# Kernel tuning notes

Hardware: AMD Instinct MI355X
Metric: run time of the kernel (lower is better)

## Reference

```python
import jax, jax.numpy as jnp
import numpy as np

NEG_BIG = 1e13  # matches the torch module's (mask-1)*1e13 additive mask


def setup_inputs() -> dict:
    key = jax.random.key(0)
    k1, k2, k3, k4 = jax.random.split(key, 4)
    B, Lq, Lk, D = 32, 1024, 1024, 1024  # D = 2*hidden = 2*embedding
    query = jax.random.normal(k1, (B, Lq, D), dtype=jnp.float32)
    key_t = jax.random.normal(k2, (B, Lk, D), dtype=jnp.float32)
    key_mask = jax.random.randint(k3, (B, Lk), 0, 2).astype(jnp.float32)
    # Linear(hidden*2 -> embedding*2): weight [out, in] torch convention
    W = jax.random.normal(k4, (D, D), dtype=jnp.float32) * (1.0 / np.sqrt(D))
    b = jnp.zeros((D,), dtype=jnp.float32)
    return {"query": query, "key": key_t, "key_mask": key_mask, "W": W, "b": b}


def reference(query, key, key_mask, W, b):
    # query_emb: Dropout (identity at eval) -> Linear -> ReLU
    query_feat = jax.nn.relu(jnp.einsum("bqd,ed->bqe", query, W) + b)  # [B,Lq,D]
    # bmm with multiplicatively masked key
    masked_key = key * key_mask[:, :, None]                             # [B,Lk,D]
    score = jnp.einsum("bqd,bkd->bqk", query_feat, masked_key)          # [B,Lq,Lk]
    # masked_softmax: score*mask + (mask-1)*1e13, softmax over last dim
    m = key_mask[:, None, :]                                            # [B,1,Lk]
    attn = jax.nn.softmax(score * m + (m - 1.0) * NEG_BIG, axis=-1)     # [B,Lq,Lk]
    # weighted sum over the UNmasked key (as in the original module)
    return jnp.einsum("bqk,bkd->bqd", attn, key)                        # [B,Lq,D]
```

## Files before the change

### kernel.cpp

```cpp
#include <hip/hip_runtime.h>
#include <hip/hip_bf16.h>


typedef __attribute__((ext_vector_type(4))) float f32x4;
typedef __attribute__((ext_vector_type(8))) short s16x8;

#define MFMA16(a, b, c) __builtin_amdgcn_mfma_f32_16x16x32_bf16((a), (b), (c), 0, 0, 0)

__device__ __forceinline__ unsigned short f2bf(float x) {
  unsigned u = __builtin_bit_cast(unsigned, x);
  return (unsigned short)((u + 0x7FFFu + ((u >> 16) & 1u)) >> 16);
}
__device__ __forceinline__ float bf2f(unsigned short h) {
  return __builtin_bit_cast(float, ((unsigned)h) << 16);
}
__device__ __forceinline__ int swz(int row, int col) {
  return (row * 64 + col) ^ ((row & 7) << 3);
}
__device__ __forceinline__ void cvt8(const float* __restrict__ s, s16x8& h8, s16x8& l8) {
  f32x4 a = *(const f32x4*)s;
  f32x4 b = *(const f32x4*)(s + 4);
#pragma unroll
  for (int i = 0; i < 8; i++) {
    float v = (i < 4) ? a[i] : b[i - 4];
    unsigned short hu = f2bf(v);
    unsigned short lu = f2bf(v - bf2f(hu));
    h8[i] = (short)hu;
    l8[i] = (short)lu;
  }
}
__device__ __forceinline__ void gld16(const void* g, void* lds) {
  __builtin_amdgcn_global_load_lds((const __attribute__((address_space(1))) unsigned int*)g,
                                   (__attribute__((address_space(3))) unsigned int*)lds, 16, 0, 0);
}

#define OFF_KHI 0ULL
#define OFF_KLO 67108864ULL
#define OFF_KHIT 134217728ULL
#define OFF_QHI 201326592ULL
#define OFF_QLO 268435456ULL
#define OFF_WHI 335544320ULL
#define OFF_WLO 337641472ULL
#define WS_TIER_A 339738624ULL
#define WS_TIER_B2 201326592ULL

__global__ __launch_bounds__(256) void k_cvt_pair(const float* __restrict__ src,
                                                  unsigned short* __restrict__ hi,
                                                  unsigned short* __restrict__ lo, int n8) {
  int i = blockIdx.x * 256 + threadIdx.x;
  if (i >= n8) return;
  s16x8 h, l;
  cvt8(src + (size_t)i * 8, h, l);
  *(s16x8*)(hi + (size_t)i * 8) = h;
  *(s16x8*)(lo + (size_t)i * 8) = l;
}

__global__ __launch_bounds__(256) void k_cvt_k(const float* __restrict__ K,
                                               unsigned short* __restrict__ Khi,
                                               unsigned short* __restrict__ Klo,
                                               unsigned short* __restrict__ KhiT) {
  __shared__ unsigned T[64 * 65];
  const int t = threadIdx.x;
  const int db0 = blockIdx.x * 64, kb0 = blockIdx.y * 64, b = blockIdx.z;
  const size_t base = (size_t)b * 1024 * 1024;
#pragma unroll
  for (int i = 0; i < 2; i++) {
    const int r = (t >> 3) + i * 32, c0 = (t & 7) * 8;
    s16x8 h, l;
    cvt8(K + base + (size_t)(kb0 + r) * 1024 + db0 + c0, h, l);
    *(s16x8*)(Khi + base + (size_t)(kb0 + r) * 1024 + db0 + c0) = h;
    *(s16x8*)(Klo + base + (size_t)(kb0 + r) * 1024 + db0 + c0) = l;
#pragma unroll
    for (int j = 0; j < 8; j++)
      T[r * 65 + c0 + j] = ((unsigned)(unsigned short)h[j] << 16) | (unsigned short)l[j];
  }
  __syncthreads();
#pragma unroll
  for (int i = 0; i < 2; i++) {
    const int rd = (t >> 3) + i * 32, ck0 = (t & 7) * 8;
    s16x8 h;
#pragma unroll
    for (int j = 0; j < 8; j++) h[j] = (short)(unsigned short)(T[(ck0 + j) * 65 + rd] >> 16);
    *(s16x8*)(KhiT + base + (size_t)(db0 + rd) * 1024 + kb0 + ck0) = h;
  }
}

__global__ __launch_bounds__(256, 2) void k_qf2(const unsigned short* __restrict__ Qhi,
                                                const unsigned short* __restrict__ Qlo,
                                                const unsigned short* __restrict__ Whi,
                                                const unsigned short* __restrict__ Wlo,
                                                const float* __restrict__ bias,
                                                float* __restrict__ outp) {
  __shared__ __align__(16) unsigned short Ah[128 * 64], Al[128 * 64], Bh[128 * 64], Bl[128 * 64];
  const int t = threadIdx.x;
  const int i = blockIdx.x + blockIdx.y * 256;
  const int x = i & 7, j = i >> 3;
  const int n0 = (j & 7) * 128;
  const int m0 = (x * 32 + (j >> 3)) * 128;
  const int w = t >> 6, l = t & 63, wm = w >> 1, wn = w & 1, g = l >> 4, ln = l & 15;
  const int lrow = l >> 3, lc8 = (l & 7) * 8;
  const f32x4 fz = {0.f, 0.f, 0.f, 0.f};
  f32x4 acc[4][4];
#pragma unroll
  for (int a = 0; a < 4; a++)
#pragma unroll
    for (int bq = 0; bq < 4; bq++) acc[a][bq] = fz;
#pragma unroll 1
  for (int k0 = 0; k0 < 1024; k0 += 64) {
#pragma unroll
    for (int jj = 0; jj < 4; jj++) {
      const int ch = w * 4 + jj;
      const int row = ch * 8 + lrow;
      const int sc = lc8 ^ (lrow << 3);
      gld16(Qhi + (size_t)(m0 + row) * 1024 + k0 + sc, &Ah[ch * 512]);
      gld16(Qlo + (size_t)(m0 + row) * 1024 + k0 + sc, &Al[ch * 512]);
      gld16(Whi + (size_t)(n0 + row) * 1024 + k0 + sc, &Bh[ch * 512]);
      gld16(Wlo + (size_t)(n0 + row) * 1024 + k0 + sc, &Bl[ch * 512]);
    }
    __syncthreads();
#pragma unroll
    for (int ks = 0; ks < 2; ks++) {
      const int kc = ks * 32 + g * 8;
      s16x8 ah[4], al[4], bh[4], bl[4];
#pragma unroll
      for (int mf = 0; mf < 4; mf++) {
        const int row = wm * 64 + mf * 16 + ln;
        const int idx = row * 64 + (kc ^ ((row & 7) << 3));
        ah[mf] = *(const s16x8*)&Ah[idx];
        al[mf] = *(const s16x8*)&Al[idx];
      }
#pragma unroll
      for (int nf = 0; nf < 4; nf++) {
        const int row = wn * 64 + nf * 16 + ln;
        const int idx = row * 64 + (kc ^ ((row & 7) << 3));
        bh[nf] = *(const s16x8*)&Bh[idx];
        bl[nf] = *(const s16x8*)&Bl[idx];
      }
#pragma unroll
      for (int mf = 0; mf < 4; mf++)
#pragma unroll
        for (int nf = 0; nf < 4; nf++) {
          acc[mf][nf] = MFMA16(ah[mf], bh[nf], acc[mf][nf]);
          acc[mf][nf] = MFMA16(ah[mf], bl[nf], acc[mf][nf]);
          acc[mf][nf] = MFMA16(al[mf], bh[nf], acc[mf][nf]);
        }
    }
    __syncthreads();
  }
  unsigned short* oc = (unsigned short*)outp;
#pragma unroll
  for (int nf = 0; nf < 4; nf++) {
    const int col = n0 + wn * 64 + nf * 16 + ln;
    const float bv = bias[col];
#pragma unroll
    for (int mf = 0; mf < 4; mf++)
#pragma unroll
      for (int r = 0; r < 4; r++) {
        const int row = m0 + wm * 64 + mf * 16 + g * 4 + r;
        float v = acc[mf][nf][r] + bv;
        v = v > 0.f ? v : 0.f;
        unsigned short h = f2bf(v);
        oc[(size_t)row * 2048 + col] = h;
        oc[(size_t)row * 2048 + 1024 + col] = f2bf(v - bf2f(h));
      }
  }
}

__global__ __launch_bounds__(512, 2) void k_attn2(const unsigned short* __restrict__ Khi,
                                                  const unsigned short* __restrict__ Klo,
                                                  const float* __restrict__ mask,
                                                  float* __restrict__ dout) {
  __shared__ __align__(16) unsigned short qh[64 * 64], ql[64 * 64], kh[128 * 64], kl[128 * 64];
  __shared__ float mask_s[1024];
  __shared__ float red[4][64];
  const int t = threadIdx.x;
  const int i = blockIdx.y * 16 + blockIdx.x;
  const int x = i & 7, jj = i >> 3;
  const int b = x * 4 + (jj >> 4), qt = jj & 15;
  const int q0 = qt * 64;
  const int w = t >> 6, l = t & 63, wm = w >> 2, wn = w & 3, g = l >> 4, ln = l & 15;
  const int lrow = l >> 3, lc8 = (l & 7) * 8, sc = lc8 ^ (lrow << 3);
  for (int ii = t; ii < 1024; ii += 512) mask_s[ii] = mask[b * 1024 + ii];
  const f32x4 fz = {0.f, 0.f, 0.f, 0.f};
  f32x4 acc[8][2][2];
#pragma unroll
  for (int kt = 0; kt < 8; kt++)
#pragma unroll
    for (int mf = 0; mf < 2; mf++)
#pragma unroll
      for (int nf = 0; nf < 2; nf++) acc[kt][mf][nf] = fz;
  const unsigned short* dou16 = (const unsigned short*)dout;
  const size_t kbase = (size_t)b * 1024 * 1024;
#pragma unroll 1
  for (int dc = 0; dc < 16; dc++) {
    {
      const int row = w * 8 + lrow;
      const unsigned short* gq = dou16 + (size_t)(b * 1024 + q0 + row) * 2048 + dc * 64 + sc;
      gld16(gq, &qh[w * 512]);
      gld16(gq + 1024, &ql[w * 512]);
    }
#pragma unroll
    for (int kt = 0; kt < 8; kt++) {
#pragma unroll
      for (int jj2 = 0; jj2 < 2; jj2++) {
        const int ch = w * 2 + jj2;
        const int row = ch * 8 + lrow;
        const size_t go = kbase + (size_t)(kt * 128 + row) * 1024 + dc * 64 + sc;
        gld16(Khi + go, &kh[ch * 512]);
        gld16(Klo + go, &kl[ch * 512]);
      }
      __syncthreads();
#pragma unroll
      for (int ks = 0; ks < 2; ks++) {
        const int kc = ks * 32 + g * 8;
        s16x8 ah[2], al2[2], bh[2], bl[2];
#pragma unroll
        for (int mf = 0; mf < 2; mf++) {
          const int row = wm * 32 + mf * 16 + ln;
          const int idx = row * 64 + (kc ^ ((row & 7) << 3));
          ah[mf] = *(const s16x8*)&qh[idx];
          al2[mf] = *(const s16x8*)&ql[idx];
        }
#pragma unroll
        for (int nf = 0; nf < 2; nf++) {
          const int row = wn * 32 + nf * 16 + ln;
          const int idx = row * 64 + (kc ^ ((row & 7) << 3));
          bh[nf] = *(const s16x8*)&kh[idx];
          bl[nf] = *(const s16x8*)&kl[idx];
        }
#pragma unroll
        for (int mf = 0; mf < 2; mf++)
#pragma unroll
          for (int nf = 0; nf < 2; nf++) {
            acc[kt][mf][nf] = MFMA16(ah[mf], bh[nf], acc[kt][mf][nf]);
            acc[kt][mf][nf] = MFMA16(ah[mf], bl[nf], acc[kt][mf][nf]);
            acc[kt][mf][nf] = MFMA16(al2[mf], bh[nf], acc[kt][mf][nf]);
          }
      }
      __syncthreads();
    }
  }
  float rmax[2][4];
#pragma unroll
  for (int mf = 0; mf < 2; mf++)
#pragma unroll
    for (int r = 0; r < 4; r++) rmax[mf][r] = -1e30f;
#pragma unroll
  for (int kt = 0; kt < 8; kt++)
#pragma unroll
    for (int nf = 0; nf < 2; nf++) {
      const int k = kt * 128 + wn * 32 + nf * 16 + ln;
      const bool mk = mask_s[k] != 0.f;
#pragma unroll
      for (int mf = 0; mf < 2; mf++)
#pragma unroll
        for (int r = 0; r < 4; r++)
          if (mk) rmax[mf][r] = fmaxf(rmax[mf][r], acc[kt][mf][nf][r]);
    }
#pragma unroll
  for (int off = 1; off < 16; off <<= 1)
#pragma unroll
    for (int mf = 0; mf < 2; mf++)
#pragma unroll
      for (int r = 0; r < 4; r++) rmax[mf][r] = fmaxf(rmax[mf][r], __shfl_xor(rmax[mf][r], off));
  if (ln == 0) {
#pragma unroll
    for (int mf = 0; mf < 2; mf++)
#pragma unroll
      for (int r = 0; r < 4; r++) red[wn][wm * 32 + mf * 16 + g * 4 + r] = rmax[mf][r];
  }
  __syncthreads();
#pragma unroll
  for (int mf = 0; mf < 2; mf++)
#pragma unroll
    for (int r = 0; r < 4; r++) {
      const int row = wm * 32 + mf * 16 + g * 4 + r;
      rmax[mf][r] = fmaxf(fmaxf(red[0][row], red[1][row]), fmaxf(red[2][row], red[3][row]));
    }
  __syncthreads();
  float rsum[2][4];
#pragma unroll
  for (int mf = 0; mf < 2; mf++)
#pragma unroll
    for (int r = 0; r < 4; r++) rsum[mf][r] = 0.f;
#pragma unroll
  for (int kt = 0; kt < 8; kt++)
#pragma unroll
    for (int nf = 0; nf < 2; nf++) {
      const int k = kt * 128 + wn * 32 + nf * 16 + ln;
      const bool mk = mask_s[k] != 0.f;
#pragma unroll
      for (int mf = 0; mf < 2; mf++)
#pragma unroll
        for (int r = 0; r < 4; r++)
          if (mk) rsum[mf][r] += __expf(acc[kt][mf][nf][r] - rmax[mf][r]);
    }
#pragma unroll
  for (int off = 1; off < 16; off <<= 1)
#pragma unroll
    for (int mf = 0; mf < 2; mf++)
#pragma unroll
      for (int r = 0; r < 4; r++) rsum[mf][r] += __shfl_xor(rsum[mf][r], off);
  if (ln == 0) {
#pragma unroll
    for (int mf = 0; mf < 2; mf++)
#pragma unroll
      for (int r = 0; r < 4; r++) red[wn][wm * 32 + mf * 16 + g * 4 + r] = rsum[mf][r];
  }
  __syncthreads();
  float rinv[2][4];
#pragma unroll
  for (int mf = 0; mf < 2; mf++)
#pragma unroll
    for (int r = 0; r < 4; r++) {
      const int row = wm * 32 + mf * 16 + g * 4 + r;
      rinv[mf][r] = 1.f / (red[0][row] + red[1][row] + red[2][row] + red[3][row]);
    }
  unsigned short* oc = (unsigned short*)dout;
#pragma unroll
  for (int kt = 0; kt < 8; kt++)
#pragma unroll
    for (int nf = 0; nf < 2; nf++) {
      const int k = kt * 128 + wn * 32 + nf * 16 + ln;
      const bool mk = mask_s[k] != 0.f;
#pragma unroll
      for (int mf = 0; mf < 2; mf++)
#pragma unroll
        for (int r = 0; r < 4; r++) {
          const int q = q0 + wm * 32 + mf * 16 + g * 4 + r;
          float p = mk ? __expf(acc[kt][mf][nf][r] - rmax[mf][r]) * rinv[mf][r] : 0.f;
          oc[(size_t)(b * 1024 + q) * 2048 + 1024 + k] = f2bf(p);
        }
    }
}

__global__ __launch_bounds__(512, 2) void k_pv2(const unsigned short* __restrict__ KhiT,
                                                float* __restrict__ dout, const int dh) {
  __shared__ __align__(16) unsigned short P[128 * 64];
  __shared__ __align__(16) unsigned short KT[512 * 64];
  const int t = threadIdx.x;
  const int i = blockIdx.y * 8 + blockIdx.x;
  const int x = i & 7, jj = i >> 3;
  const int b = x * 4 + (jj >> 3), qt = jj & 7;
  const int q0 = qt * 128, d0 = dh * 512;
  const int w = t >> 6, l = t & 63, wm = w >> 2, wd = w & 3, g = l >> 4, ln = l & 15;
  const int lrow = l >> 3, lc8 = (l & 7) * 8, sc = lc8 ^ (lrow << 3);
  const f32x4 fz = {0.f, 0.f, 0.f, 0.f};
  f32x4 acc[4][8];
#pragma unroll
  for (int a = 0; a < 4; a++)
#pragma unroll
    for (int bq = 0; bq < 8; bq++) acc[a][bq] = fz;
  const unsigned short* dou16 = (const unsigned short*)dout;
  const size_t kbase = (size_t)b * 1024 * 1024;
#pragma unroll 1
  for (int k0 = 0; k0 < 1024; k0 += 64) {
#pragma unroll
    for (int jj2 = 0; jj2 < 2; jj2++) {
      const int ch = w * 2 + jj2;
      const int row = ch * 8 + lrow;
      gld16(dou16 + (size_t)(b * 1024 + q0 + row) * 2048 + 1024 + k0 + sc, &P[ch * 512]);
    }
#pragma unroll
    for (int jj2 = 0; jj2 < 8; jj2++) {
      const int ch = w * 8 + jj2;
      const int row = ch * 8 + lrow;
      gld16(KhiT + kbase + (size_t)(d0 + row) * 1024 + k0 + sc, &KT[ch * 512]);
    }
    __syncthreads();
#pragma unroll
    for (int ks = 0; ks < 2; ks++) {
      const int kc = ks * 32 + g * 8;
      s16x8 a[4], bb[8];
#pragma unroll
      for (int mf = 0; mf < 4; mf++) {
        const int row = wm * 64 + mf * 16 + ln;
        a[mf] = *(const s16x8*)&P[row * 64 + (kc ^ ((row & 7) << 3))];
      }
#pragma unroll
      for (int nf = 0; nf < 8; nf++) {
        const int row = wd * 128 + nf * 16 + ln;
        bb[nf] = *(const s16x8*)&KT[row * 64 + (kc ^ ((row & 7) << 3))];
      }
#pragma unroll
      for (int mf = 0; mf < 4; mf++)
#pragma unroll
        for (int nf = 0; nf < 8; nf++) acc[mf][nf] = MFMA16(a[mf], bb[nf], acc[mf][nf]);
    }
    __syncthreads();
  }
#pragma unroll
  for (int mf = 0; mf < 4; mf++)
#pragma unroll
    for (int nf = 0; nf < 8; nf++)
#pragma unroll
      for (int r = 0; r < 4; r++) {
        const int q = q0 + wm * 64 + mf * 16 + g * 4 + r;
        const int d = d0 + wd * 128 + nf * 16 + ln;
        dout[(size_t)(b * 1024 + q) * 1024 + d] = acc[mf][nf][r];
      }
}

__global__ __launch_bounds__(256, 2) void k_qf(const float* __restrict__ Q,
                                               const float* __restrict__ W,
                                               const float* __restrict__ bias,
                                               float* __restrict__ qf, const int packout) {
  __shared__ __align__(16) short Ah[128 * 64], Al[128 * 64], Bh[128 * 64], Bl[128 * 64];
  const int t = threadIdx.x;
  const int m0 = blockIdx.x * 128, n0 = blockIdx.y * 128;
  const int w = t >> 6, l = t & 63, wm = w >> 1, wn = w & 1, g = l >> 4, ln = l & 15;
  const f32x4 fz = {0.f, 0.f, 0.f, 0.f};
  f32x4 acc[4][4];
#pragma unroll
  for (int a = 0; a < 4; a++)
#pragma unroll
    for (int bq = 0; bq < 4; bq++) acc[a][bq] = fz;
  const int srow = t >> 1, scol = (t & 1) * 32;
#pragma unroll 1
  for (int k0 = 0; k0 < 1024; k0 += 64) {
    const float* sa = Q + (size_t)(m0 + srow) * 1024 + k0 + scol;
    const float* sb = W + (size_t)(n0 + srow) * 1024 + k0 + scol;
#pragma unroll
    for (int c = 0; c < 32; c += 8) {
      s16x8 h, lo;
      cvt8(sa + c, h, lo);
      int si = swz(srow, scol + c);
      *(s16x8*)&Ah[si] = h;
      *(s16x8*)&Al[si] = lo;
    }
#pragma unroll
    for (int c = 0; c < 32; c += 8) {
      s16x8 h, lo;
      cvt8(sb + c, h, lo);
      int si = swz(srow, scol + c);
      *(s16x8*)&Bh[si] = h;
      *(s16x8*)&Bl[si] = lo;
    }
    __syncthreads();
#pragma unroll
    for (int ks = 0; ks < 2; ks++) {
      const int kc = ks * 32 + g * 8;
      s16x8 ah[4], al[4], bh[4], bl[4];
#pragma unroll
      for (int mf = 0; mf < 4; mf++) {
        int si = swz(wm * 64 + mf * 16 + ln, kc);
        ah[mf] = *(s16x8*)&Ah[si];
        al[mf] = *(s16x8*)&Al[si];
      }
#pragma unroll
      for (int nf = 0; nf < 4; nf++) {
        int si = swz(wn * 64 + nf * 16 + ln, kc);
        bh[nf] = *(s16x8*)&Bh[si];
        bl[nf] = *(s16x8*)&Bl[si];
      }
#pragma unroll
      for (int mf = 0; mf < 4; mf++)
#pragma unroll
        for (int nf = 0; nf < 4; nf++) {
          acc[mf][nf] = MFMA16(ah[mf], bh[nf], acc[mf][nf]);
          acc[mf][nf] = MFMA16(ah[mf], bl[nf], acc[mf][nf]);
          acc[mf][nf] = MFMA16(al[mf], bh[nf], acc[mf][nf]);
        }
    }
    __syncthreads();
  }
  unsigned short* oc = (unsigned short*)qf;
#pragma unroll
  for (int nf = 0; nf < 4; nf++) {
    const int col = n0 + wn * 64 + nf * 16 + ln;
    const float bv = bias[col];
#pragma unroll
    for (int mf = 0; mf < 4; mf++)
#pragma unroll
      for (int r = 0; r < 4; r++) {
        const int row = m0 + wm * 64 + mf * 16 + g * 4 + r;
        float v = acc[mf][nf][r] + bv;
        v = v > 0.f ? v : 0.f;
        if (packout) {
          unsigned short h = f2bf(v);
          oc[(size_t)row * 2048 + col] = h;
          oc[(size_t)row * 2048 + 1024 + col] = f2bf(v - bf2f(h));
        } else {
          qf[(size_t)row * 1024 + col] = v;
        }
      }
  }
}

__global__ __launch_bounds__(512, 2) void k_attn(const float* __restrict__ Key,
                                                 const float* __restrict__ mask,
                                                 float* __restrict__ dout) {
  __shared__ __align__(16) short qh[64 * 64], qlo[64 * 64], kh[128 * 64], klo[128 * 64];
  __shared__ float mask_s[1024];
  __shared__ float red[4][64];
  const int t = threadIdx.x;
  const int qt = blockIdx.x, b = blockIdx.y;
  const int q0 = qt * 64;
  const int w = t >> 6, l = t & 63, wm = w >> 2, wn = w & 3, g = l >> 4, ln = l & 15;
  for (int i = t; i < 1024; i += 512) mask_s[i] = mask[b * 1024 + i];
  const f32x4 fz = {0.f, 0.f, 0.f, 0.f};
  f32x4 acc[8][2][2];
#pragma unroll
  for (int kt = 0; kt < 8; kt++)
#pragma unroll
    for (int mf = 0; mf < 2; mf++)
#pragma unroll
      for (int nf = 0; nf < 2; nf++) acc[kt][mf][nf] = fz;
  const float* qfb = dout + (size_t)(b * 1024 + q0) * 1024;
  const float* kb = Key + (size_t)b * 1024 * 1024;
  const int qrow = t >> 3, qcol = (t & 7) * 8;
  const int krow = t >> 2, kcol0 = (t & 3) * 16;
#pragma unroll 1
  for (int dc = 0; dc < 16; dc++) {
    {
      s16x8 h, lo;
      cvt8(qfb + (size_t)qrow * 1024 + dc * 64 + qcol, h, lo);
      int si = swz(qrow, qcol);
      *(s16x8*)&qh[si] = h;
      *(s16x8*)&qlo[si] = lo;
    }
#pragma unroll
    for (int kt = 0; kt < 8; kt++) {
      {
        const float* s = kb + (size_t)(kt * 128 + krow) * 1024 + dc * 64 + kcol0;
        s16x8 h, lo;
        cvt8(s, h, lo);
        int si = swz(krow, kcol0);
        *(s16x8*)&kh[si] = h;
        *(s16x8*)&klo[si] = lo;
        cvt8(s + 8, h, lo);
        si = swz(krow, kcol0 + 8);
        *(s16x8*)&kh[si] = h;
        *(s16x8*)&klo[si] = lo;
      }
      __syncthreads();
#pragma unroll
      for (int ks = 0; ks < 2; ks++) {
        const int kc = ks * 32 + g * 8;
        s16x8 ah[2], al2[2], bh[2], bl[2];
#pragma unroll
        for (int mf = 0; mf < 2; mf++) {
          int si = swz(wm * 32 + mf * 16 + ln, kc);
          ah[mf] = *(s16x8*)&qh[si];
          al2[mf] = *(s16x8*)&qlo[si];
        }
#pragma unroll
        for (int nf = 0; nf < 2; nf++) {
          int si = swz(wn * 32 + nf * 16 + ln, kc);
          bh[nf] = *(s16x8*)&kh[si];
          bl[nf] = *(s16x8*)&klo[si];
        }
#pragma unroll
        for (int mf = 0; mf < 2; mf++)
#pragma unroll
          for (int nf = 0; nf < 2; nf++) {
            acc[kt][mf][nf] = MFMA16(ah[mf], bh[nf], acc[kt][mf][nf]);
            acc[kt][mf][nf] = MFMA16(ah[mf], bl[nf], acc[kt][mf][nf]);
            acc[kt][mf][nf] = MFMA16(al2[mf], bh[nf], acc[kt][mf][nf]);
          }
      }
      __syncthreads();
    }
  }
  float rmax[2][4];
#pragma unroll
  for (int mf = 0; mf < 2; mf++)
#pragma unroll
    for (int r = 0; r < 4; r++) rmax[mf][r] = -1e30f;
#pragma unroll
  for (int kt = 0; kt < 8; kt++)
#pragma unroll
    for (int nf = 0; nf < 2; nf++) {
      const int k = kt * 128 + wn * 32 + nf * 16 + ln;
      const bool mk = mask_s[k] != 0.f;
#pragma unroll
      for (int mf = 0; mf < 2; mf++)
#pragma unroll
        for (int r = 0; r < 4; r++)
          if (mk) rmax[mf][r] = fmaxf(rmax[mf][r], acc[kt][mf][nf][r]);
    }
#pragma unroll
  for (int off = 1; off < 16; off <<= 1)
#pragma unroll
    for (int mf = 0; mf < 2; mf++)
#pragma unroll
      for (int r = 0; r < 4; r++) rmax[mf][r] = fmaxf(rmax[mf][r], __shfl_xor(rmax[mf][r], off));
  if (ln == 0) {
#pragma unroll
    for (int mf = 0; mf < 2; mf++)
#pragma unroll
      for (int r = 0; r < 4; r++) red[wn][wm * 32 + mf * 16 + g * 4 + r] = rmax[mf][r];
  }
  __syncthreads();
#pragma unroll
  for (int mf = 0; mf < 2; mf++)
#pragma unroll
    for (int r = 0; r < 4; r++) {
      const int row = wm * 32 + mf * 16 + g * 4 + r;
      rmax[mf][r] = fmaxf(fmaxf(red[0][row], red[1][row]), fmaxf(red[2][row], red[3][row]));
    }
  __syncthreads();
  float rsum[2][4];
#pragma unroll
  for (int mf = 0; mf < 2; mf++)
#pragma unroll
    for (int r = 0; r < 4; r++) rsum[mf][r] = 0.f;
#pragma unroll
  for (int kt = 0; kt < 8; kt++)
#pragma unroll
    for (int nf = 0; nf < 2; nf++) {
      const int k = kt * 128 + wn * 32 + nf * 16 + ln;
      const bool mk = mask_s[k] != 0.f;
#pragma unroll
      for (int mf = 0; mf < 2; mf++)
#pragma unroll
        for (int r = 0; r < 4; r++)
          if (mk) rsum[mf][r] += __expf(acc[kt][mf][nf][r] - rmax[mf][r]);
    }
#pragma unroll
  for (int off = 1; off < 16; off <<= 1)
#pragma unroll
    for (int mf = 0; mf < 2; mf++)
#pragma unroll
      for (int r = 0; r < 4; r++) rsum[mf][r] += __shfl_xor(rsum[mf][r], off);
  if (ln == 0) {
#pragma unroll
    for (int mf = 0; mf < 2; mf++)
#pragma unroll
      for (int r = 0; r < 4; r++) red[wn][wm * 32 + mf * 16 + g * 4 + r] = rsum[mf][r];
  }
  __syncthreads();
  float rinv[2][4];
#pragma unroll
  for (int mf = 0; mf < 2; mf++)
#pragma unroll
    for (int r = 0; r < 4; r++) {
      const int row = wm * 32 + mf * 16 + g * 4 + r;
      rinv[mf][r] = 1.f / (red[0][row] + red[1][row] + red[2][row] + red[3][row]);
    }
  char* oc = (char*)dout;
#pragma unroll
  for (int kt = 0; kt < 8; kt++)
#pragma unroll
    for (int nf = 0; nf < 2; nf++) {
      const int k = kt * 128 + wn * 32 + nf * 16 + ln;
      const bool mk = mask_s[k] != 0.f;
#pragma unroll
      for (int mf = 0; mf < 2; mf++)
#pragma unroll
        for (int r = 0; r < 4; r++) {
          const int q = q0 + wm * 32 + mf * 16 + g * 4 + r;
          float p = mk ? __expf(acc[kt][mf][nf][r] - rmax[mf][r]) * rinv[mf][r] : 0.f;
          *(unsigned short*)(oc + (size_t)(b * 1024 + q) * 4096 + 2048 + k * 2) = f2bf(p);
        }
    }
}

__global__ __launch_bounds__(512, 2) void k_pv(const float* __restrict__ Key,
                                               float* __restrict__ dout, const int dh) {
  __shared__ __align__(16) short P[128 * 64];
  __shared__ __align__(16) short KT[512 * 64];
  const int t = threadIdx.x;
  const int qt = blockIdx.x, b = blockIdx.y;
  const int q0 = qt * 128, d0 = dh * 512;
  const int w = t >> 6, l = t & 63, wm = w >> 2, wd = w & 3, g = l >> 4, ln = l & 15;
  const f32x4 fz = {0.f, 0.f, 0.f, 0.f};
  f32x4 acc[4][8];
#pragma unroll
  for (int a = 0; a < 4; a++)
#pragma unroll
    for (int bq = 0; bq < 8; bq++) acc[a][bq] = fz;
  const char* ab = (const char*)dout;
  const int prow = t >> 2, pc0 = (t & 3) * 16;
#pragma unroll 1
  for (int k0 = 0; k0 < 1024; k0 += 64) {
    {
      const unsigned short* s =
          (const unsigned short*)(ab + (size_t)(b * 1024 + q0 + prow) * 4096 + 2048) + k0 + pc0;
      s16x8 p0 = *(const s16x8*)s, p1 = *(const s16x8*)(s + 8);
      *(s16x8*)&P[swz(prow, pc0)] = p0;
      *(s16x8*)&P[swz(prow, pc0 + 8)] = p1;
    }
    {
      const float* ksrc = Key + (size_t)b * 1024 * 1024 + (size_t)k0 * 1024 + d0 + t;
#pragma unroll
      for (int kg = 0; kg < 8; kg++) {
        s16x8 h;
#pragma unroll
        for (int jx = 0; jx < 8; jx++) h[jx] = (short)f2bf(ksrc[(size_t)(kg * 8 + jx) * 1024]);
        *(s16x8*)&KT[swz(t, kg * 8)] = h;
      }
    }
    __syncthreads();
#pragma unroll
    for (int ks = 0; ks < 2; ks++) {
      const int kc = ks * 32 + g * 8;
      s16x8 a[4], bb[8];
#pragma unroll
      for (int mf = 0; mf < 4; mf++) a[mf] = *(s16x8*)&P[swz(wm * 64 + mf * 16 + ln, kc)];
#pragma unroll
      for (int nf = 0; nf < 8; nf++) bb[nf] = *(s16x8*)&KT[swz(wd * 128 + nf * 16 + ln, kc)];
#pragma unroll
      for (int mf = 0; mf < 4; mf++)
#pragma unroll
        for (int nf = 0; nf < 8; nf++) acc[mf][nf] = MFMA16(a[mf], bb[nf], acc[mf][nf]);
    }
    __syncthreads();
  }
#pragma unroll
  for (int mf = 0; mf < 4; mf++)
#pragma unroll
    for (int nf = 0; nf < 8; nf++)
#pragma unroll
      for (int r = 0; r < 4; r++) {
        const int q = q0 + wm * 64 + mf * 16 + g * 4 + r;
        const int d = d0 + wd * 128 + nf * 16 + ln;
        dout[(size_t)(b * 1024 + q) * 1024 + d] = acc[mf][nf][r];
      }
}

extern "C" void kernel_launch(void* const* d_in, const int* in_sizes, int n_in,
                              void* d_out, int out_size, void* d_ws, size_t ws_size,
                              hipStream_t stream) {
  const float* Q = (const float*)d_in[0];
  const float* K = (const float*)d_in[1];
  const float* M = (const float*)d_in[2];
  const float* W = (const float*)d_in[3];
  const float* bias = (const float*)d_in[4];
  float* out = (float*)d_out;
  char* wsb = (char*)d_ws;
  (void)in_sizes; (void)n_in; (void)out_size;

  const bool tierA = ws_size >= WS_TIER_A;
  const bool tierB2 = !tierA && ws_size >= WS_TIER_B2;
  if (tierA || tierB2) {
    unsigned short* Khi = (unsigned short*)(wsb + OFF_KHI);
    unsigned short* Klo = (unsigned short*)(wsb + OFF_KLO);
    unsigned short* KhiT = (unsigned short*)(wsb + OFF_KHIT);
    k_cvt_k<<<dim3(16, 16, 32), 256, 0, stream>>>(K, Khi, Klo, KhiT);
    if (tierA) {
      unsigned short* Qhi = (unsigned short*)(wsb + OFF_QHI);
      unsigned short* Qlo = (unsigned short*)(wsb + OFF_QLO);
      unsigned short* Whi = (unsigned short*)(wsb + OFF_WHI);
      unsigned short* Wlo = (unsigned short*)(wsb + OFF_WLO);
      k_cvt_pair<<<16384, 256, 0, stream>>>(Q, Qhi, Qlo, 4194304);
      k_cvt_pair<<<512, 256, 0, stream>>>(W, Whi, Wlo, 131072);
      k_qf2<<<dim3(256, 8), 256, 0, stream>>>(Qhi, Qlo, Whi, Wlo, bias, out);
    } else {
      k_qf<<<dim3(256, 8), 256, 0, stream>>>(Q, W, bias, out, 1);
    }
    k_attn2<<<dim3(16, 32), 512, 0, stream>>>(Khi, Klo, M, out);
    k_pv2<<<dim3(8, 32), 512, 0, stream>>>(KhiT, out, 0);
    k_pv2<<<dim3(8, 32), 512, 0, stream>>>(KhiT, out, 1);
  } else {
    k_qf<<<dim3(256, 8), 256, 0, stream>>>(Q, W, bias, out, 0);
    k_attn<<<dim3(16, 32), 512, 0, stream>>>(K, M, out);
    k_pv<<<dim3(8, 32), 512, 0, stream>>>(K, out, 0);
    k_pv<<<dim3(8, 32), 512, 0, stream>>>(K, out, 1);
  }
}
```

Baseline: 820.0 us.

## Double-buffer K tiles in LDS and load Q fragments directly into registers

Replaces the single K tile buffer in the score-GEMM phase of k_attn2 with a two-stage LDS double buffer, so the next K chunk is issued before computing on the current one and one barrier per step is dropped. Q hi/lo fragments are now read straight from global memory into registers for each d-chunk instead of being staged through shared memory. This overlaps global K loads with MFMA work and removes Q's LDS traffic, but doubles K's LDS footprint and adds register pressure. With launch bounds of 2 blocks of 512 threads and 128 accumulator registers already held, this could hurt occupancy or cause spills.

```diff
diff --git a/kernel.cpp b/kernel.cpp
--- a/kernel.cpp
+++ b/kernel.cpp
@@ -170,7 +170,7 @@
                                                   const unsigned short* __restrict__ Klo,
                                                   const float* __restrict__ mask,
                                                   float* __restrict__ dout) {
-  __shared__ __align__(16) unsigned short qh[64 * 64], ql[64 * 64], kh[128 * 64], kl[128 * 64];
+  __shared__ __align__(16) unsigned short kbuf[2][2][128 * 64];
   __shared__ float mask_s[1024];
   __shared__ float red[4][64];
   const int t = threadIdx.x;
@@ -191,53 +191,62 @@
       for (int nf = 0; nf < 2; nf++) acc[kt][mf][nf] = fz;
   const unsigned short* dou16 = (const unsigned short*)dout;
   const size_t kbase = (size_t)b * 1024 * 1024;
+
+  auto stageK = [&](int buf, int kt, int dc) {
+#pragma unroll
+    for (int jj2 = 0; jj2 < 2; jj2++) {
+      const int ch = w * 2 + jj2;
+      const int row = ch * 8 + lrow;
+      const size_t go = kbase + (size_t)(kt * 128 + row) * 1024 + dc * 64 + sc;
+      gld16(Khi + go, &kbuf[buf][0][ch * 512]);
+      gld16(Klo + go, &kbuf[buf][1][ch * 512]);
+    }
+  };
+
+  stageK(0, 0, 0);
+  __syncthreads();
+  int cur = 0;
 #pragma unroll 1
   for (int dc = 0; dc < 16; dc++) {
-    {
-      const int row = w * 8 + lrow;
-      const unsigned short* gq = dou16 + (size_t)(b * 1024 + q0 + row) * 2048 + dc * 64 + sc;
-      gld16(gq, &qh[w * 512]);
-      gld16(gq + 1024, &ql[w * 512]);
-    }
+    s16x8 qh[2][2], ql[2][2];
+#pragma unroll
+    for (int mf = 0; mf < 2; mf++)
+#pragma unroll
+      for (int ks = 0; ks < 2; ks++) {
+        const size_t rowoff = (size_t)(b * 1024 + q0 + wm * 32 + mf * 16 + ln) * 2048;
+        const int col = dc * 64 + ks * 32 + g * 8;
+        qh[mf][ks] = *(const s16x8*)(dou16 + rowoff + col);
+        ql[mf][ks] = *(const s16x8*)(dou16 + rowoff + 1024 + col);
+      }
 #pragma unroll
     for (int kt = 0; kt < 8; kt++) {
-#pragma unroll
-      for (int jj2 = 0; jj2 < 2; jj2++) {
-        const int ch = w * 2 + jj2;
-        const int row = ch * 8 + lrow;
-        const size_t go = kbase + (size_t)(kt * 128 + row) * 1024 + dc * 64 + sc;
-        gld16(Khi + go, &kh[ch * 512]);
-        gld16(Klo + go, &kl[ch * 512]);
-      }
-      __syncthreads();
+      if (!(dc == 15 && kt == 7)) {
+        const int nkt = (kt + 1) & 7;
+        const int ndc = (kt == 7) ? dc + 1 : dc;
+        stageK(cur ^ 1, nkt, ndc);
+      }
 #pragma unroll
       for (int ks = 0; ks < 2; ks++) {
         const int kc = ks * 32 + g * 8;
-        s16x8 ah[2], al2[2], bh[2], bl[2];
-#pragma unroll
-        for (int mf = 0; mf < 2; mf++) {
-          const int row = wm * 32 + mf * 16 + ln;
-          const int idx = row * 64 + (kc ^ ((row & 7) << 3));
-          ah[mf] = *(const s16x8*)&qh[idx];
-          al2[mf] = *(const s16x8*)&ql[idx];
-        }
+        s16x8 bh[2], bl[2];
 #pragma unroll
         for (int nf = 0; nf < 2; nf++) {
           const int row = wn * 32 + nf * 16 + ln;
           const int idx = row * 64 + (kc ^ ((row & 7) << 3));
-          bh[nf] = *(const s16x8*)&kh[idx];
-          bl[nf] = *(const s16x8*)&kl[idx];
+          bh[nf] = *(const s16x8*)&kbuf[cur][0][idx];
+          bl[nf] = *(const s16x8*)&kbuf[cur][1][idx];
         }
 #pragma unroll
         for (int mf = 0; mf < 2; mf++)
 #pragma unroll
           for (int nf = 0; nf < 2; nf++) {
-            acc[kt][mf][nf] = MFMA16(ah[mf], bh[nf], acc[kt][mf][nf]);
-            acc[kt][mf][nf] = MFMA16(ah[mf], bl[nf], acc[kt][mf][nf]);
-            acc[kt][mf][nf] = MFMA16(al2[mf], bh[nf], acc[kt][mf][nf]);
+            acc[kt][mf][nf] = MFMA16(qh[mf][ks], bh[nf], acc[kt][mf][nf]);
+            acc[kt][mf][nf] = MFMA16(qh[mf][ks], bl[nf], acc[kt][mf][nf]);
+            acc[kt][mf][nf] = MFMA16(ql[mf][ks], bh[nf], acc[kt][mf][nf]);
           }
       }
       __syncthreads();
+      cur ^= 1;
     }
   }
   float rmax[2][4];
```

After: 801.0 us. 1.02x faster.
